# Kernel tuning notes

Measured on AMD Instinct MI355X. Metric: run time of the kernel, lower is better.

## Reference

```python
import jax, jax.numpy as jnp
import numpy as np

B, S, D = 2, 2048, 2048
H, KVH = 16, 4
HD = D // H          # 128 head dim
KVD = KVH * HD       # 512
BASE = 10000.0
EPS = 1.1920929e-07  # float32 eps, matches torch F.rms_norm default


def setup_inputs() -> dict:
    key = jax.random.key(0)
    ks = jax.random.split(key, 9)
    sd = 1.0 / np.sqrt(D)
    x = jax.random.normal(ks[0], (B, S, D), jnp.float32)
    Wq = jax.random.normal(ks[1], (D, D), jnp.float32) * sd
    bq = jnp.zeros((D,), jnp.float32)
    Wk = jax.random.normal(ks[2], (KVD, D), jnp.float32) * sd
    bk = jnp.zeros((KVD,), jnp.float32)
    Wv = jax.random.normal(ks[3], (KVD, D), jnp.float32) * sd
    bv = jnp.zeros((KVD,), jnp.float32)
    Wo = jax.random.normal(ks[4], (D, D), jnp.float32) * sd
    bo = jnp.zeros((D,), jnp.float32)
    q_gain = jnp.ones((H,), jnp.float32)
    return {"x": x, "Wq": Wq, "bq": bq, "Wk": Wk, "bk": bk,
            "Wv": Wv, "bv": bv, "Wo": Wo, "bo": bo, "q_gain": q_gain}


def _rms_norm(t):
    return t * jax.lax.rsqrt(jnp.mean(t * t, axis=-1, keepdims=True) + EPS)


def _rope_tables(s, dtype):
    inv_freq = 1.0 / (BASE ** (jnp.arange(0, HD, 2, dtype=jnp.float32) / HD))  # [HD/2]
    t = jnp.arange(s, dtype=jnp.float32)
    freqs = jnp.outer(t, inv_freq)                       # [s, HD/2]
    cos = jnp.cos(freqs)[None, None].astype(dtype)       # [1,1,s,HD/2]
    sin = jnp.sin(freqs)[None, None].astype(dtype)
    return cos, sin


def _apply_rope(t, cos, sin):
    half = t.shape[-1] // 2
    t1, t2 = t[..., :half], t[..., half:]
    return jnp.concatenate([t1 * cos + t2 * sin, -t1 * sin + t2 * cos], axis=-1)


def reference(x, Wq, bq, Wk, bk, Wv, bv, Wo, bo, q_gain):
    b, s, d = x.shape
    q = (jnp.einsum('bsd,ed->bse', x, Wq) + bq).reshape(b, s, H, HD).transpose(0, 2, 1, 3)
    k = (jnp.einsum('bsd,ed->bse', x, Wk) + bk).reshape(b, s, KVH, HD).transpose(0, 2, 1, 3)
    v = (jnp.einsum('bsd,ed->bse', x, Wv) + bv).reshape(b, s, KVH, HD).transpose(0, 2, 1, 3)
    # QK RMSNorm (no learned weight)
    q = _rms_norm(q)
    k = _rms_norm(k)
    # RoPE over full head dim (rope_dims=0 path)
    cos, sin = _rope_tables(s, q.dtype)
    q = _apply_rope(q, cos, sin)
    k = _apply_rope(k, cos, sin)
    # per-head gain on q
    q = q * q_gain[None, :, None, None]
    # GQA: repeat kv heads
    rep = H // KVH
    k = jnp.repeat(k, rep, axis=1)
    v = jnp.repeat(v, rep, axis=1)
    scale = HD ** -0.5
    attn = jnp.einsum('bhqd,bhkd->bhqk', q * scale, k)   # [b,H,s,s]
    causal = jnp.tril(jnp.ones((s, s), dtype=bool))
    attn = jnp.where(causal[None, None], attn, -jnp.inf)
    attn = jax.nn.softmax(attn, axis=-1)
    out = jnp.einsum('bhqk,bhkd->bqhd', attn, v).reshape(b, s, d)
    return jnp.einsum('bsd,ed->bse', out, Wo) + bo
```

## Files before the change

kernel.cpp:

```cpp
#include <hip/hip_runtime.h>
#include <hip/hip_bf16.h>

typedef __hip_bfloat16 bf16;
typedef unsigned short u16;
typedef short short8 __attribute__((ext_vector_type(8)));
typedef float f32x4  __attribute__((ext_vector_type(4)));

static __device__ __forceinline__ float ldf(const void* p, size_t i, int isbf16) {
    return isbf16 ? __bfloat162float(((const bf16*)p)[i]) : ((const float*)p)[i];
}
static __device__ __forceinline__ void stf(void* p, size_t i, float v, int isbf16) {
    if (isbf16) ((bf16*)p)[i] = __float2bfloat16(v);
    else        ((float*)p)[i] = v;
}

static __device__ __forceinline__ unsigned packf(float v) {
    unsigned ub = __float_as_uint(v);
    unsigned uh = ub & 0xFFFF0000u;
    float r = v - __uint_as_float(uh);
    return uh | (__float_as_uint(r) >> 16);
}
static __device__ __forceinline__ float unpackf(unsigned u) {
    return __uint_as_float(u & 0xFFFF0000u) + __uint_as_float(u << 16);
}

static __device__ __forceinline__ void upk8(uint4 a, uint4 b, short8& h, short8& l) {
    h = (short8){(short)(a.x >> 16), (short)(a.y >> 16), (short)(a.z >> 16), (short)(a.w >> 16),
                 (short)(b.x >> 16), (short)(b.y >> 16), (short)(b.z >> 16), (short)(b.w >> 16)};
    l = (short8){(short)(a.x), (short)(a.y), (short)(a.z), (short)(a.w),
                 (short)(b.x), (short)(b.y), (short)(b.z), (short)(b.w)};
}

static __device__ __forceinline__ void splitf8(float4 a, float4 b, short8& h, short8& l) {
    float vv[8] = {a.x, a.y, a.z, a.w, b.x, b.y, b.z, b.w};
    unsigned hh[8], ll[8];
#pragma unroll
    for (int j = 0; j < 8; j++) {
        unsigned ub = __float_as_uint(vv[j]);
        unsigned uh = ub & 0xFFFF0000u;
        float r = vv[j] - __uint_as_float(uh);
        hh[j] = uh >> 16;
        ll[j] = __float_as_uint(r) >> 16;
    }
    h = (short8){(short)hh[0], (short)hh[1], (short)hh[2], (short)hh[3],
                 (short)hh[4], (short)hh[5], (short)hh[6], (short)hh[7]};
    l = (short8){(short)ll[0], (short)ll[1], (short)ll[2], (short)ll[3],
                 (short)ll[4], (short)ll[5], (short)ll[6], (short)ll[7]};
}

static __device__ __forceinline__ float4 u2f4(uint4 a) {
    return (float4){__uint_as_float(a.x), __uint_as_float(a.y),
                    __uint_as_float(a.z), __uint_as_float(a.w)};
}
static __device__ __forceinline__ short8 u4_s8(uint4 a) {
    return (short8){(short)(a.x & 0xFFFF), (short)(a.x >> 16),
                    (short)(a.y & 0xFFFF), (short)(a.y >> 16),
                    (short)(a.z & 0xFFFF), (short)(a.z >> 16),
                    (short)(a.w & 0xFFFF), (short)(a.w >> 16)};
}

template<int AK>
static __device__ __forceinline__ void load_raw(const void* P, size_t e, int f, uint4* r) {
    if (AK == 1) {
        const uint4* p = (const uint4*)((const unsigned*)P + e);
        r[0] = p[0]; r[1] = p[1]; r[2] = p[2]; r[3] = p[3];
    } else if (f == 0) {
        const uint4* p = (const uint4*)((const float*)P + e);
        r[0] = p[0]; r[1] = p[1]; r[2] = p[2]; r[3] = p[3];
    } else {
        const uint4* p = (const uint4*)((const u16*)P + e);
        r[0] = p[0]; r[1] = p[1];
        r[2] = (uint4){0, 0, 0, 0}; r[3] = (uint4){0, 0, 0, 0};
    }
}

template<int AK>
static __device__ __forceinline__ void conv_raw(const uint4* r, int f,
        short8& h0, short8& h1, short8& l0, short8& l1) {
    if (AK == 1) {
        upk8(r[0], r[1], h0, l0);
        upk8(r[2], r[3], h1, l1);
    } else if (f == 0) {
        splitf8(u2f4(r[0]), u2f4(r[1]), h0, l0);
        splitf8(u2f4(r[2]), u2f4(r[3]), h1, l1);
    } else {
        h0 = u4_s8(r[0]); h1 = u4_s8(r[1]);
        l0 = (short8){0,0,0,0,0,0,0,0};
        l1 = (short8){0,0,0,0,0,0,0,0};
    }
}

__global__ void detect_dtype(const unsigned short* __restrict__ x, int n, int* __restrict__ flag)
{
    __shared__ int cnt;
    if (threadIdx.x == 0) cnt = 0;
    __syncthreads();
    int local = 0;
    for (int i = threadIdx.x; i < n; i += blockDim.x) {
        const unsigned int e = (x[i] >> 7) & 0xFF;
        if (e >= 134u) local++;
    }
    atomicAdd(&cnt, local);
    __syncthreads();
    if (threadIdx.x == 0) *flag = (cnt >= 32) ? 0 : 1;
}

template<int AK, int OUT, int BROW>
static __device__ __forceinline__ void gemm_core(
    const void* __restrict__ A, const void* __restrict__ W,
    const void* __restrict__ bias, void* __restrict__ C,
    int M, int N, int K, int f, int bx, int by, u16* sm)
{
    u16* Ah = sm;
    u16* Al = sm + 4096;
    u16* Wh = sm + 8192;
    u16* Wl = sm + 12288;

    const int t = threadIdx.x;
    const int w = t >> 6, lane = t & 63;
    const int wm = w >> 1, wn = w & 1;
    const int lr = lane & 15, quad = lane >> 4;
    const int bm = by * 128, bn = bx * 128;
    const int srow = t >> 1;
    const int scol = (t & 1) * 16;

    f32x4 acc[4][4];
#pragma unroll
    for (int i = 0; i < 4; i++)
#pragma unroll
        for (int j = 0; j < 4; j++) acc[i][j] = (f32x4){0.f, 0.f, 0.f, 0.f};

    uint4 ar[4], wr2[4];
    const size_t abase = (size_t)(bm + srow) * K + scol;
    const size_t wbase = (size_t)(bn + srow) * K + scol;
    load_raw<AK>(A, abase, f, ar);
    load_raw<0>(W, wbase, f, wr2);

    for (int k0 = 0; k0 < K; k0 += 32) {
        __syncthreads();
        {
            short8 h0, h1, l0, l1;
            conv_raw<AK>(ar, f, h0, h1, l0, l1);
            const int o = srow * 32 + scol;
            *(short8*)&Ah[o] = h0; *(short8*)&Ah[o + 8] = h1;
            *(short8*)&Al[o] = l0; *(short8*)&Al[o + 8] = l1;
            conv_raw<0>(wr2, f, h0, h1, l0, l1);
            *(short8*)&Wh[o] = h0; *(short8*)&Wh[o + 8] = h1;
            *(short8*)&Wl[o] = l0; *(short8*)&Wl[o + 8] = l1;
        }
        __syncthreads();
        if (k0 + 32 < K) {
            load_raw<AK>(A, abase + k0 + 32, f, ar);
            load_raw<0>(W, wbase + k0 + 32, f, wr2);
        }

        short8 avh[4], avl[4], bvh[4], bvl[4];
#pragma unroll
        for (int i = 0; i < 4; i++) {
            const int o = (wm * 64 + i * 16 + lr) * 32 + quad * 8;
            avh[i] = *(const short8*)&Ah[o];
            avl[i] = *(const short8*)&Al[o];
        }
#pragma unroll
        for (int j = 0; j < 4; j++) {
            const int o = (wn * 64 + j * 16 + lr) * 32 + quad * 8;
            bvh[j] = *(const short8*)&Wh[o];
            bvl[j] = *(const short8*)&Wl[o];
        }
        __builtin_amdgcn_s_setprio(1);
#pragma unroll
        for (int i = 0; i < 4; i++)
#pragma unroll
            for (int j = 0; j < 4; j++) {
                acc[i][j] = __builtin_amdgcn_mfma_f32_16x16x32_bf16(avl[i], bvh[j], acc[i][j], 0, 0, 0);
                acc[i][j] = __builtin_amdgcn_mfma_f32_16x16x32_bf16(avh[i], bvl[j], acc[i][j], 0, 0, 0);
                acc[i][j] = __builtin_amdgcn_mfma_f32_16x16x32_bf16(avh[i], bvh[j], acc[i][j], 0, 0, 0);
            }
        __builtin_amdgcn_s_setprio(0);
    }

#pragma unroll
    for (int j = 0; j < 4; j++) {
        const int col = bn + wn * 64 + j * 16 + lr;
        const float bc = BROW ? 0.f : ldf(bias, col, f);
#pragma unroll
        for (int i = 0; i < 4; i++) {
            const int row0 = bm + wm * 64 + i * 16 + quad * 4;
#pragma unroll
            for (int r = 0; r < 4; r++) {
                const int row = row0 + r;
                const float bb = BROW ? ldf(bias, row, f) : bc;
                const float val = acc[i][j][r] + bb;
                if (OUT == 1) ((unsigned*)C)[(size_t)row * N + col] = packf(val);
                else          stf(C, (size_t)row * N + col, val, f);
            }
        }
    }
}

template<int AK, int OUT, int BROW>
__global__ __launch_bounds__(256, 2)
void gemm3(const void* __restrict__ A, const void* __restrict__ W,
           const void* __restrict__ bias, void* __restrict__ C,
           int M, int N, int K, const int* __restrict__ flagp)
{
    extern __shared__ u16 sm[];
    gemm_core<AK, OUT, BROW>(A, W, bias, C, M, N, K, *flagp, blockIdx.x, blockIdx.y, sm);
}

__global__ __launch_bounds__(256, 2)
void gemm_kv(const void* __restrict__ x,
             const void* __restrict__ Wk, const void* __restrict__ bk, unsigned* __restrict__ Kp,
             const void* __restrict__ Wv, const void* __restrict__ bv, unsigned* __restrict__ Vtp,
             const int* __restrict__ flagp)
{
    extern __shared__ u16 sm[];
    const int f = *flagp;
    if (blockIdx.x < 4)
        gemm_core<0, 1, 0>(x, Wk, bk, Kp, 4096, 512, 2048, f, blockIdx.x, blockIdx.y, sm);
    else
        gemm_core<0, 1, 1>(Wv, x, bv, Vtp, 512, 4096, 2048, f, blockIdx.y, blockIdx.x - 4, sm);
}

__global__ __launch_bounds__(64)
void norm_rope_pk(unsigned* __restrict__ buf, const void* __restrict__ gain,
                  int nheads, float scale, const int* __restrict__ flagp)
{
    const int id = blockIdx.x;
    const int h  = id % nheads;
    const int bs = id / nheads;
    const int s  = bs & 2047;
    unsigned* v = buf + (size_t)bs * nheads * 128 + h * 128;
    const int i = threadIdx.x;

    float t1 = unpackf(v[i]);
    float t2 = unpackf(v[i + 64]);
    float ss = t1 * t1 + t2 * t2;
#pragma unroll
    for (int off = 32; off >= 1; off >>= 1) ss += __shfl_xor(ss, off);
    const float r = rsqrtf(ss * (1.0f / 128.0f) + 1.1920929e-07f);
    t1 *= r; t2 *= r;

    const float inv_freq = exp2f(-(float)i * 0.20762050593046014f);
    const float ph = (float)s * inv_freq;
    float sn, cs;
    __sincosf(ph, &sn, &cs);

    float g = scale;
    if (gain) g *= ldf(gain, h, *flagp);

    v[i]      = packf((t1 * cs + t2 * sn) * g);
    v[i + 64] = packf((-t1 * sn + t2 * cs) * g);
}

__global__ __launch_bounds__(256, 2)
void attn3(const unsigned* __restrict__ Qp, const unsigned* __restrict__ Kp,
           const unsigned* __restrict__ Vtp, unsigned* __restrict__ Cp)
{
    const int S = 2048, D = 2048, KVD = 512, MT = 4096;

    __shared__ __align__(16) u16 Kh[64 * 128], Kl[64 * 128];
    __shared__ __align__(16) u16 Vh[128 * 64], Vl[128 * 64];
    __shared__ __align__(16) u16 Ps[4][16][72];

    const int t = threadIdx.x, w = t >> 6, lane = t & 63;
    const int lr = lane & 15, quad = lane >> 4;
    const int h = blockIdx.y, b = blockIdx.z;
    const int kvh = h >> 2;

    const int qt0 = blockIdx.x;
    const int qt1 = 31 - blockIdx.x;
    const int nt0 = qt0 + 1, nt1 = qt1 + 1;
    const int total = nt0 + nt1;

    const int kr = t >> 2, kq = t & 3;
    const int vd = t >> 1, vh2 = t & 1;
    const unsigned* kg = Kp + (size_t)(b * S + kr) * KVD + kvh * 128 + kq * 32;
    const unsigned* vg = Vtp + (size_t)(kvh * 128 + vd) * MT + b * S + vh2 * 32;
    char* KhB = (char*)Kh; char* KlB = (char*)Kl;
    char* VhB = (char*)Vh; char* VlB = (char*)Vl;

    uint4 kv[8], vv[8];
#define ISSUE_KV(K0)                                                     \
    do {                                                                 \
        _Pragma("unroll")                                                \
        for (int u = 0; u < 8; u++) {                                    \
            kv[u] = *(const uint4*)(kg + (size_t)(K0) * KVD + u * 4);    \
            vv[u] = *(const uint4*)(vg + (K0) + u * 4);                  \
        }                                                                \
    } while (0)

    short8 qh[4], ql[4];
    f32x4 acc[8];
    float mreg[4], lreg[4];
    int q0 = 0, nt = nt0;

    ISSUE_KV(0);

    for (int it = 0; it < total; it++) {
        const int item = (it >= nt0) ? 1 : 0;
        const int kt = item ? (it - nt0) : it;
        if (kt == 0) {
            nt = item ? nt1 : nt0;
            q0 = (item ? qt1 : qt0) * 64;
            const unsigned* qs = Qp + (size_t)(b * S + q0 + w * 16 + lr) * D + h * 128;
#pragma unroll
            for (int kk = 0; kk < 4; kk++) {
                const uint4* p = (const uint4*)(qs + kk * 32 + quad * 8);
                upk8(p[0], p[1], qh[kk], ql[kk]);
            }
#pragma unroll
            for (int dt = 0; dt < 8; dt++) acc[dt] = (f32x4){0.f, 0.f, 0.f, 0.f};
#pragma unroll
            for (int r = 0; r < 4; r++) { mreg[r] = -1e30f; lreg[r] = 0.f; }
        }
        const int k0 = kt * 64;

        __syncthreads();
#pragma unroll
        for (int u2 = 0; u2 < 4; u2++) {
            short8 hh, ll;
            upk8(kv[2 * u2], kv[2 * u2 + 1], hh, ll);
            const int ko = (kr * 256 + kq * 64 + u2 * 16) ^ ((kr & 7) << 4);
            *(short8*)(KhB + ko) = hh;
            *(short8*)(KlB + ko) = ll;
            upk8(vv[2 * u2], vv[2 * u2 + 1], hh, ll);
            const int vo = (vd * 128 + vh2 * 64 + u2 * 16) ^ ((vd & 7) << 4);
            *(short8*)(VhB + vo) = hh;
            *(short8*)(VlB + vo) = ll;
        }
        __syncthreads();

        if (it + 1 < total) {
            const int nk0 = (it + 1 >= nt0) ? (it + 1 - nt0) * 64 : (it + 1) * 64;
            ISSUE_KV(nk0);
        }

        f32x4 sacc[4];
#pragma unroll
        for (int ct = 0; ct < 4; ct++) sacc[ct] = (f32x4){0.f, 0.f, 0.f, 0.f};
#pragma unroll
        for (int ks = 0; ks < 4; ks++) {
            short8 kbh[4], kbl[4];
#pragma unroll
            for (int ct = 0; ct < 4; ct++) {
                const int row = ct * 16 + lr;
                const int off = (row * 256 + ks * 64 + quad * 16) ^ ((row & 7) << 4);
                kbh[ct] = *(const short8*)(KhB + off);
                kbl[ct] = *(const short8*)(KlB + off);
            }
            __builtin_amdgcn_s_setprio(1);
#pragma unroll
            for (int ct = 0; ct < 4; ct++) {
                sacc[ct] = __builtin_amdgcn_mfma_f32_16x16x32_bf16(ql[ks], kbh[ct], sacc[ct], 0, 0, 0);
                sacc[ct] = __builtin_amdgcn_mfma_f32_16x16x32_bf16(qh[ks], kbl[ct], sacc[ct], 0, 0, 0);
                sacc[ct] = __builtin_amdgcn_mfma_f32_16x16x32_bf16(qh[ks], kbh[ct], sacc[ct], 0, 0, 0);
            }
            __builtin_amdgcn_s_setprio(0);
        }

        const bool diag = (kt == nt - 1);
        float p[4][4];
#pragma unroll
        for (int r = 0; r < 4; r++) {
            const int qg = q0 + w * 16 + quad * 4 + r;
            float s0 = sacc[0][r], s1 = sacc[1][r], s2 = sacc[2][r], s3 = sacc[3][r];
            if (diag) {
                if (k0 +  0 + lr > qg) s0 = -1e30f;
                if (k0 + 16 + lr > qg) s1 = -1e30f;
                if (k0 + 32 + lr > qg) s2 = -1e30f;
                if (k0 + 48 + lr > qg) s3 = -1e30f;
            }
            float mt = fmaxf(fmaxf(s0, s1), fmaxf(s2, s3));
#pragma unroll
            for (int off = 1; off < 16; off <<= 1) mt = fmaxf(mt, __shfl_xor(mt, off));
            const float mnew  = fmaxf(mreg[r], mt);
            const float alpha = __expf(mreg[r] - mnew);
            p[r][0] = (s0 <= -1e29f) ? 0.f : __expf(s0 - mnew);
            p[r][1] = (s1 <= -1e29f) ? 0.f : __expf(s1 - mnew);
            p[r][2] = (s2 <= -1e29f) ? 0.f : __expf(s2 - mnew);
            p[r][3] = (s3 <= -1e29f) ? 0.f : __expf(s3 - mnew);
            float ps = p[r][0] + p[r][1] + p[r][2] + p[r][3];
#pragma unroll
            for (int off = 1; off < 16; off <<= 1) ps += __shfl_xor(ps, off);
            lreg[r] = lreg[r] * alpha + ps;
            mreg[r] = mnew;
#pragma unroll
            for (int dt = 0; dt < 8; dt++) acc[dt][r] *= alpha;
        }

#pragma unroll
        for (int r = 0; r < 4; r++)
#pragma unroll
            for (int ct = 0; ct < 4; ct++)
                Ps[w][quad * 4 + r][ct * 16 + lr] = (u16)(__float_as_uint(p[r][ct]) >> 16);
#pragma unroll
        for (int ks2 = 0; ks2 < 2; ks2++) {
            const short8 pa = *(const short8*)((const char*)&Ps[w][lr][0] + ks2 * 64 + quad * 16);
            __builtin_amdgcn_s_setprio(1);
#pragma unroll
            for (int dt = 0; dt < 8; dt++) {
                const int vrow = dt * 16 + lr;
                const int off = (vrow * 128 + ks2 * 64 + quad * 16) ^ ((vrow & 7) << 4);
                const short8 vbh = *(const short8*)(VhB + off);
                const short8 vbl = *(const short8*)(VlB + off);
                acc[dt] = __builtin_amdgcn_mfma_f32_16x16x32_bf16(pa, vbh, acc[dt], 0, 0, 0);
                acc[dt] = __builtin_amdgcn_mfma_f32_16x16x32_bf16(pa, vbl, acc[dt], 0, 0, 0);
            }
            __builtin_amdgcn_s_setprio(0);
        }
#pragma unroll
        for (int r = 0; r < 4; r++)
#pragma unroll
            for (int ct = 0; ct < 4; ct++) {
                const unsigned ub = __float_as_uint(p[r][ct]);
                const unsigned uh = ub & 0xFFFF0000u;
                const float rr = p[r][ct] - __uint_as_float(uh);
                Ps[w][quad * 4 + r][ct * 16 + lr] = (u16)(__float_as_uint(rr) >> 16);
            }
#pragma unroll
        for (int ks2 = 0; ks2 < 2; ks2++) {
            const short8 pa = *(const short8*)((const char*)&Ps[w][lr][0] + ks2 * 64 + quad * 16);
            __builtin_amdgcn_s_setprio(1);
#pragma unroll
            for (int dt = 0; dt < 8; dt++) {
                const int vrow = dt * 16 + lr;
                const int off = (vrow * 128 + ks2 * 64 + quad * 16) ^ ((vrow & 7) << 4);
                const short8 vbh = *(const short8*)(VhB + off);
                acc[dt] = __builtin_amdgcn_mfma_f32_16x16x32_bf16(pa, vbh, acc[dt], 0, 0, 0);
            }
            __builtin_amdgcn_s_setprio(0);
        }

        if (kt == nt - 1) {
#pragma unroll
            for (int r = 0; r < 4; r++) {
                const float inv = 1.0f / lreg[r];
                unsigned* dst = Cp + (size_t)(b * S + q0 + w * 16 + quad * 4 + r) * D + h * 128 + lr;
#pragma unroll
                for (int dt = 0; dt < 8; dt++)
                    dst[dt * 16] = packf(acc[dt][r] * inv);
            }
        }
    }
#undef ISSUE_KV
}

extern "C" void kernel_launch(void* const* d_in, const int* in_sizes, int n_in,
                              void* d_out, int out_size, void* d_ws, size_t ws_size,
                              hipStream_t stream)
{
    const void* x  = d_in[0];
    const void* Wq = d_in[1];
    const void* bq = d_in[2];
    const void* Wk = d_in[3];
    const void* bk = d_in[4];
    const void* Wv = d_in[5];
    const void* bv = d_in[6];
    const void* Wo = d_in[7];
    const void* bo = d_in[8];
    const void* qg = d_in[9];

    const int B = 2, S = 2048, D = 2048, H = 16, KVH = 4, KVD = 512;
    const int M = B * S;

    unsigned* Qp  = (unsigned*)d_ws;
    unsigned* Kp  = Qp + (size_t)M * D;
    unsigned* Vtp = Kp + (size_t)M * KVD;
    unsigned* Cp  = Vtp + (size_t)KVD * M;
    int* flag = (int*)(Cp + (size_t)M * D);

    detect_dtype<<<1, 256, 0, stream>>>((const unsigned short*)x, 16384, flag);

    gemm3<0, 1, 0><<<dim3(D / 128, M / 128), 256, 32768, stream>>>(
        x, Wq, bq, Qp, M, D, D, flag);
    gemm_kv<<<dim3(8, 32), 256, 32768, stream>>>(x, Wk, bk, Kp, Wv, bv, Vtp, flag);

    norm_rope_pk<<<M * H, 64, 0, stream>>>(Qp, qg, H, 0.08838834764831845f, flag);
    norm_rope_pk<<<M * KVH, 64, 0, stream>>>(Kp, nullptr, KVH, 1.0f, flag);

    attn3<<<dim3(16, H, B), 256, 0, stream>>>(Qp, Kp, Vtp, Cp);

    gemm3<1, 2, 0><<<dim3(D / 128, M / 128), 256, 32768, stream>>>(
        Cp, Wo, bo, d_out, M, D, D, flag);
}
```

Before: 716.4 us.

## Pre-split activations into bf16 hi/lo planes and stream them with async LDS copies

Adds a split_x pass that converts x once into separate bf16 high and low planes. The Q, K and V projections are merged into one launch whose pre-split operand is copied straight into shared memory with global_load_lds, so it is no longer converted per tile in every block. K, V and the attention output are stored as planar hi/lo bf16 arrays instead of packed words, which lets attention and the output GEMM copy them without unpacking. This removes repeated fp32-to-bf16x2 splitting and register staging, at the cost of an extra pass over x and more workspace; the GEMMs now claim 3 blocks per SM through launch bounds.

Result: slower. 889.8 us (+24.2%).

```diff
diff --git a/kernel.cpp b/kernel.cpp
--- a/kernel.cpp
+++ b/kernel.cpp
@@ -5,6 +5,10 @@
 typedef unsigned short u16;
 typedef short short8 __attribute__((ext_vector_type(8)));
 typedef float f32x4  __attribute__((ext_vector_type(4)));
+
+static __device__ __forceinline__ float b2f(u16 u) {
+    union { unsigned int i; float f; } c; c.i = (unsigned int)u << 16; return c.f;
+}
 
 static __device__ __forceinline__ float ldf(const void* p, size_t i, int isbf16) {
     return isbf16 ? __bfloat162float(((const bf16*)p)[i]) : ((const float*)p)[i];
@@ -59,12 +63,8 @@
                     (short)(a.w & 0xFFFF), (short)(a.w >> 16)};
 }
 
-template<int AK>
 static __device__ __forceinline__ void load_raw(const void* P, size_t e, int f, uint4* r) {
-    if (AK == 1) {
-        const uint4* p = (const uint4*)((const unsigned*)P + e);
-        r[0] = p[0]; r[1] = p[1]; r[2] = p[2]; r[3] = p[3];
-    } else if (f == 0) {
+    if (f == 0) {
         const uint4* p = (const uint4*)((const float*)P + e);
         r[0] = p[0]; r[1] = p[1]; r[2] = p[2]; r[3] = p[3];
     } else {
@@ -73,14 +73,9 @@
         r[2] = (uint4){0, 0, 0, 0}; r[3] = (uint4){0, 0, 0, 0};
     }
 }
-
-template<int AK>
 static __device__ __forceinline__ void conv_raw(const uint4* r, int f,
         short8& h0, short8& h1, short8& l0, short8& l1) {
-    if (AK == 1) {
-        upk8(r[0], r[1], h0, l0);
-        upk8(r[2], r[3], h1, l1);
-    } else if (f == 0) {
+    if (f == 0) {
         splitf8(u2f4(r[0]), u2f4(r[1]), h0, l0);
         splitf8(u2f4(r[2]), u2f4(r[3]), h1, l1);
     } else {
@@ -88,6 +83,11 @@
         l0 = (short8){0,0,0,0,0,0,0,0};
         l1 = (short8){0,0,0,0,0,0,0,0};
     }
+}
+
+static __device__ __forceinline__ void async_copy16(const void* g, void* l) {
+    __builtin_amdgcn_global_load_lds((const __attribute__((address_space(1))) void*)g,
+                                     (__attribute__((address_space(3))) void*)l, 16, 0, 0);
 }
 
 __global__ void detect_dtype(const unsigned short* __restrict__ x, int n, int* __restrict__ flag)
@@ -105,24 +105,44 @@
     if (threadIdx.x == 0) *flag = (cnt >= 32) ? 0 : 1;
 }
 
-template<int AK, int OUT, int BROW>
+__global__ __launch_bounds__(256)
+void split_x(const void* __restrict__ x, u16* __restrict__ Xh, u16* __restrict__ Xl,
+             const int* __restrict__ flagp)
+{
+    const int f = *flagp;
+    const size_t i = ((size_t)blockIdx.x * 256 + threadIdx.x) * 8;
+    if (f == 0) {
+        const float4* p = (const float4*)((const float*)x + i);
+        short8 h, l;
+        splitf8(p[0], p[1], h, l);
+        *(short8*)(Xh + i) = h;
+        *(short8*)(Xl + i) = l;
+    } else {
+        *(short8*)(Xh + i) = *(const short8*)((const u16*)x + i);
+        *(short8*)(Xl + i) = (short8){0,0,0,0,0,0,0,0};
+    }
+}
+
+template<int AP, int BP, int OUT, int BROW>
 static __device__ __forceinline__ void gemm_core(
-    const void* __restrict__ A, const void* __restrict__ W,
-    const void* __restrict__ bias, void* __restrict__ C,
-    int M, int N, int K, int f, int bx, int by, u16* sm)
-{
-    u16* Ah = sm;
-    u16* Al = sm + 4096;
-    u16* Wh = sm + 8192;
-    u16* Wl = sm + 12288;
+    const void* __restrict__ Aa, const void* __restrict__ Ab,
+    const void* __restrict__ Ba, const void* __restrict__ Bb,
+    const void* __restrict__ bias, void* __restrict__ Ca, void* __restrict__ Cb,
+    int N, int K, int f, int bx, int by, u16* sm)
+{
+    u16* AhT = sm;
+    u16* AlT = sm + 4096;
+    u16* WhT = sm + 8192;
+    u16* WlT = sm + 12288;
 
     const int t = threadIdx.x;
     const int w = t >> 6, lane = t & 63;
     const int wm = w >> 1, wn = w & 1;
     const int lr = lane & 15, quad = lane >> 4;
     const int bm = by * 128, bn = bx * 128;
-    const int srow = t >> 1;
-    const int scol = (t & 1) * 16;
+    const int arow = lane >> 2;
+    const int acol = (lane & 3) * 8;
+    const int srow = t >> 1, scol = (t & 1) * 16;
 
     f32x4 acc[4][4];
 #pragma unroll
@@ -130,42 +150,54 @@
 #pragma unroll
         for (int j = 0; j < 4; j++) acc[i][j] = (f32x4){0.f, 0.f, 0.f, 0.f};
 
-    uint4 ar[4], wr2[4];
-    const size_t abase = (size_t)(bm + srow) * K + scol;
-    const size_t wbase = (size_t)(bn + srow) * K + scol;
-    load_raw<AK>(A, abase, f, ar);
-    load_raw<0>(W, wbase, f, wr2);
+    uint4 rr[4];
+    const void* rawP = AP ? Ba : Aa;
+    const size_t rawBase = AP ? ((size_t)(bn + srow) * K + scol)
+                              : ((size_t)(bm + srow) * K + scol);
+    load_raw(rawP, rawBase, f, rr);
 
     for (int k0 = 0; k0 < K; k0 += 32) {
         __syncthreads();
+        if (AP) {
+#pragma unroll
+            for (int c = 2 * w; c < 2 * w + 2; c++) {
+                const int row = c * 16 + arow;
+                async_copy16((const u16*)Aa + (size_t)(bm + row) * K + k0 + acol, &AhT[c * 512]);
+                async_copy16((const u16*)Ab + (size_t)(bm + row) * K + k0 + acol, &AlT[c * 512]);
+            }
+        }
+        if (BP) {
+#pragma unroll
+            for (int c = 2 * w; c < 2 * w + 2; c++) {
+                const int row = c * 16 + arow;
+                async_copy16((const u16*)Ba + (size_t)(bn + row) * K + k0 + acol, &WhT[c * 512]);
+                async_copy16((const u16*)Bb + (size_t)(bn + row) * K + k0 + acol, &WlT[c * 512]);
+            }
+        }
         {
             short8 h0, h1, l0, l1;
-            conv_raw<AK>(ar, f, h0, h1, l0, l1);
+            conv_raw(rr, f, h0, h1, l0, l1);
+            u16* H = AP ? WhT : AhT;
+            u16* L = AP ? WlT : AlT;
             const int o = srow * 32 + scol;
-            *(short8*)&Ah[o] = h0; *(short8*)&Ah[o + 8] = h1;
-            *(short8*)&Al[o] = l0; *(short8*)&Al[o + 8] = l1;
-            conv_raw<0>(wr2, f, h0, h1, l0, l1);
-            *(short8*)&Wh[o] = h0; *(short8*)&Wh[o + 8] = h1;
-            *(short8*)&Wl[o] = l0; *(short8*)&Wl[o + 8] = l1;
+            *(short8*)&H[o] = h0; *(short8*)&H[o + 8] = h1;
+            *(short8*)&L[o] = l0; *(short8*)&L[o + 8] = l1;
         }
         __syncthreads();
-        if (k0 + 32 < K) {
-            load_raw<AK>(A, abase + k0 + 32, f, ar);
-            load_raw<0>(W, wbase + k0 + 32, f, wr2);
-        }
+        if (k0 + 32 < K) load_raw(rawP, rawBase + k0 + 32, f, rr);
 
         short8 avh[4], avl[4], bvh[4], bvl[4];
 #pragma unroll
         for (int i = 0; i < 4; i++) {
             const int o = (wm * 64 + i * 16 + lr) * 32 + quad * 8;
-            avh[i] = *(const short8*)&Ah[o];
-            avl[i] = *(const short8*)&Al[o];
+            avh[i] = *(const short8*)&AhT[o];
+            avl[i] = *(const short8*)&AlT[o];
         }
 #pragma unroll
         for (int j = 0; j < 4; j++) {
             const int o = (wn * 64 + j * 16 + lr) * 32 + quad * 8;
-            bvh[j] = *(const short8*)&Wh[o];
-            bvl[j] = *(const short8*)&Wl[o];
+            bvh[j] = *(const short8*)&WhT[o];
+            bvl[j] = *(const short8*)&WlT[o];
         }
         __builtin_amdgcn_s_setprio(1);
 #pragma unroll
@@ -191,35 +223,54 @@
                 const int row = row0 + r;
                 const float bb = BROW ? ldf(bias, row, f) : bc;
                 const float val = acc[i][j][r] + bb;
-                if (OUT == 1) ((unsigned*)C)[(size_t)row * N + col] = packf(val);
-                else          stf(C, (size_t)row * N + col, val, f);
-            }
-        }
-    }
-}
-
-template<int AK, int OUT, int BROW>
-__global__ __launch_bounds__(256, 2)
-void gemm3(const void* __restrict__ A, const void* __restrict__ W,
-           const void* __restrict__ bias, void* __restrict__ C,
-           int M, int N, int K, const int* __restrict__ flagp)
-{
-    extern __shared__ u16 sm[];
-    gemm_core<AK, OUT, BROW>(A, W, bias, C, M, N, K, *flagp, blockIdx.x, blockIdx.y, sm);
-}
-
-__global__ __launch_bounds__(256, 2)
-void gemm_kv(const void* __restrict__ x,
-             const void* __restrict__ Wk, const void* __restrict__ bk, unsigned* __restrict__ Kp,
-             const void* __restrict__ Wv, const void* __restrict__ bv, unsigned* __restrict__ Vtp,
-             const int* __restrict__ flagp)
-{
-    extern __shared__ u16 sm[];
+                const size_t idx = (size_t)row * N + col;
+                if (OUT == 1)      ((unsigned*)Ca)[idx] = packf(val);
+                else if (OUT == 2) stf(Ca, idx, val, f);
+                else {
+                    const unsigned ub = __float_as_uint(val);
+                    const unsigned uh = ub & 0xFFFF0000u;
+                    ((u16*)Ca)[idx] = (u16)(uh >> 16);
+                    ((u16*)Cb)[idx] = (u16)(__float_as_uint(val - __uint_as_float(uh)) >> 16);
+                }
+            }
+        }
+    }
+}
+
+__global__ __launch_bounds__(256, 3)
+void gemm_qkv(const u16* __restrict__ Xh, const u16* __restrict__ Xl,
+              const void* __restrict__ Wq, const void* __restrict__ bq, unsigned* __restrict__ Qp,
+              const void* __restrict__ Wk, const void* __restrict__ bk,
+              u16* __restrict__ Khg, u16* __restrict__ Klg,
+              const void* __restrict__ Wv, const void* __restrict__ bv,
+              u16* __restrict__ Vthg, u16* __restrict__ Vtlg,
+              const int* __restrict__ flagp)
+{
+    __shared__ __align__(16) u16 sm[16384];
     const int f = *flagp;
-    if (blockIdx.x < 4)
-        gemm_core<0, 1, 0>(x, Wk, bk, Kp, 4096, 512, 2048, f, blockIdx.x, blockIdx.y, sm);
-    else
-        gemm_core<0, 1, 1>(Wv, x, bv, Vtp, 512, 4096, 2048, f, blockIdx.y, blockIdx.x - 4, sm);
+    const int id = blockIdx.x;
+    if (id < 512) {
+        gemm_core<1, 0, 1, 0>(Xh, Xl, Wq, nullptr, bq, Qp, nullptr,
+                              2048, 2048, f, id & 15, id >> 4, sm);
+    } else if (id < 640) {
+        const int v = id - 512;
+        gemm_core<1, 0, 3, 0>(Xh, Xl, Wk, nullptr, bk, Khg, Klg,
+                              512, 2048, f, v & 3, v >> 2, sm);
+    } else {
+        const int v = id - 640;
+        gemm_core<0, 1, 3, 1>(Wv, nullptr, Xh, Xl, bv, Vthg, Vtlg,
+                              4096, 2048, f, v >> 2, v & 3, sm);
+    }
+}
+
+__global__ __launch_bounds__(256, 3)
+void gemm_o(const u16* __restrict__ Ch, const u16* __restrict__ Cl,
+            const void* __restrict__ Wo, const void* __restrict__ bo,
+            void* __restrict__ out, const int* __restrict__ flagp)
+{
+    __shared__ __align__(16) u16 sm[16384];
+    gemm_core<1, 0, 2, 0>(Ch, Cl, Wo, nullptr, bo, out, nullptr,
+                          2048, 2048, *flagp, blockIdx.x & 15, blockIdx.x >> 4, sm);
 }
 
 __global__ __launch_bounds__(64)
@@ -253,9 +304,46 @@
     v[i + 64] = packf((-t1 * sn + t2 * cs) * g);
 }
 
+__global__ __launch_bounds__(64)
+void norm_rope_pl(u16* __restrict__ bh, u16* __restrict__ bl, int nheads)
+{
+    const int id = blockIdx.x;
+    const int h  = id % nheads;
+    const int bs = id / nheads;
+    const int s  = bs & 2047;
+    const size_t base = (size_t)bs * nheads * 128 + h * 128;
+    u16* ph = bh + base;
+    u16* pl = bl + base;
+    const int i = threadIdx.x;
+
+    float t1 = b2f(ph[i]) + b2f(pl[i]);
+    float t2 = b2f(ph[i + 64]) + b2f(pl[i + 64]);
+    float ss = t1 * t1 + t2 * t2;
+#pragma unroll
+    for (int off = 32; off >= 1; off >>= 1) ss += __shfl_xor(ss, off);
+    const float r = rsqrtf(ss * (1.0f / 128.0f) + 1.1920929e-07f);
+    t1 *= r; t2 *= r;
+
+    const float inv_freq = exp2f(-(float)i * 0.20762050593046014f);
+    const float phs = (float)s * inv_freq;
+    float sn, cs;
+    __sincosf(phs, &sn, &cs);
+
+    const float o1 = t1 * cs + t2 * sn;
+    const float o2 = -t1 * sn + t2 * cs;
+    unsigned u1 = __float_as_uint(o1) & 0xFFFF0000u;
+    unsigned u2 = __float_as_uint(o2) & 0xFFFF0000u;
+    ph[i]      = (u16)(u1 >> 16);
+    pl[i]      = (u16)(__float_as_uint(o1 - __uint_as_float(u1)) >> 16);
+    ph[i + 64] = (u16)(u2 >> 16);
+    pl[i + 64] = (u16)(__float_as_uint(o2 - __uint_as_float(u2)) >> 16);
+}
+
 __global__ __launch_bounds__(256, 2)
-void attn3(const unsigned* __restrict__ Qp, const unsigned* __restrict__ Kp,
-           const unsigned* __restrict__ Vtp, unsigned* __restrict__ Cp)
+void attn3(const unsigned* __restrict__ Qp,
+           const u16* __restrict__ Khg, const u16* __restrict__ Klg,
+           const u16* __restrict__ Vthg, const u16* __restrict__ Vtlg,
+           u16* __restrict__ Chg, u16* __restrict__ Clg)
 {
     const int S = 2048, D = 2048, KVD = 512, MT = 4096;
 
@@ -275,19 +363,25 @@
 
     const int kr = t >> 2, kq = t & 3;
     const int vd = t >> 1, vh2 = t & 1;
-    const unsigned* kg = Kp + (size_t)(b * S + kr) * KVD + kvh * 128 + kq * 32;
-    const unsigned* vg = Vtp + (size_t)(kvh * 128 + vd) * MT + b * S + vh2 * 32;
+    const size_t koff = (size_t)(b * S + kr) * KVD + kvh * 128 + kq * 32;
+    const size_t voff = (size_t)(kvh * 128 + vd) * MT + b * S + vh2 * 32;
+    const u16* khg = Khg + koff;
+    const u16* klg = Klg + koff;
+    const u16* vhg = Vthg + voff;
+    const u16* vlg = Vtlg + voff;
     char* KhB = (char*)Kh; char* KlB = (char*)Kl;
     char* VhB = (char*)Vh; char* VlB = (char*)Vl;
 
-    uint4 kv[8], vv[8];
-#define ISSUE_KV(K0)                                                     \
-    do {                                                                 \
-        _Pragma("unroll")                                                \
-        for (int u = 0; u < 8; u++) {                                    \
-            kv[u] = *(const uint4*)(kg + (size_t)(K0) * KVD + u * 4);    \
-            vv[u] = *(const uint4*)(vg + (K0) + u * 4);                  \
-        }                                                                \
+    uint4 khr[4], klr[4], vhr[4], vlr[4];
+#define ISSUE_KV(K0)                                                      \
+    do {                                                                  \
+        _Pragma("unroll")                                                 \
+        for (int u = 0; u < 4; u++) {                                     \
+            khr[u] = *(const uint4*)(khg + (size_t)(K0) * KVD + u * 8);   \
+            klr[u] = *(const uint4*)(klg + (size_t)(K0) * KVD + u * 8);   \
+            vhr[u] = *(const uint4*)(vhg + (K0) + u * 8);                 \
+            vlr[u] = *(const uint4*)(vlg + (K0) + u * 8);                 \
+        }                                                                 \
     } while (0)
 
     short8 qh[4], ql[4];
@@ -319,15 +413,12 @@
         __syncthreads();
 #pragma unroll
         for (int u2 = 0; u2 < 4; u2++) {
-            short8 hh, ll;
-            upk8(kv[2 * u2], kv[2 * u2 + 1], hh, ll);
             const int ko = (kr * 256 + kq * 64 + u2 * 16) ^ ((kr & 7) << 4);
-            *(short8*)(KhB + ko) = hh;
-            *(short8*)(KlB + ko) = ll;
-            upk8(vv[2 * u2], vv[2 * u2 + 1], hh, ll);
+            *(uint4*)(KhB + ko) = khr[u2];
+            *(uint4*)(KlB + ko) = klr[u2];
             const int vo = (vd * 128 + vh2 * 64 + u2 * 16) ^ ((vd & 7) << 4);
-            *(short8*)(VhB + vo) = hh;
-            *(short8*)(VlB + vo) = ll;
+            *(uint4*)(VhB + vo) = vhr[u2];
+            *(uint4*)(VlB + vo) = vlr[u2];
         }
         __syncthreads();
 
@@ -436,10 +527,15 @@
 #pragma unroll
             for (int r = 0; r < 4; r++) {
                 const float inv = 1.0f / lreg[r];
-                unsigned* dst = Cp + (size_t)(b * S + q0 + w * 16 + quad * 4 + r) * D + h * 128 + lr;
-#pragma unroll
-                for (int dt = 0; dt < 8; dt++)
-                    dst[dt * 16] = packf(acc[dt][r] * inv);
+                const size_t base = (size_t)(b * S + q0 + w * 16 + quad * 4 + r) * D + h * 128 + lr;
+#pragma unroll
+                for (int dt = 0; dt < 8; dt++) {
+                    const float val = acc[dt][r] * inv;
+                    const unsigned ub = __float_as_uint(val);
+                    const unsigned uh = ub & 0xFFFF0000u;
+                    Chg[base + dt * 16] = (u16)(uh >> 16);
+                    Clg[base + dt * 16] = (u16)(__float_as_uint(val - __uint_as_float(uh)) >> 16);
+                }
             }
         }
     }
@@ -464,23 +560,27 @@
     const int B = 2, S = 2048, D = 2048, H = 16, KVH = 4, KVD = 512;
     const int M = B * S;
 
-    unsigned* Qp  = (unsigned*)d_ws;
-    unsigned* Kp  = Qp + (size_t)M * D;
-    unsigned* Vtp = Kp + (size_t)M * KVD;
-    unsigned* Cp  = Vtp + (size_t)KVD * M;
-    int* flag = (int*)(Cp + (size_t)M * D);
+    unsigned* Qp = (unsigned*)d_ws;
+    u16* Khg  = (u16*)(Qp + (size_t)M * D);
+    u16* Klg  = Khg + (size_t)M * KVD;
+    u16* Vthg = Klg + (size_t)M * KVD;
+    u16* Vtlg = Vthg + (size_t)M * KVD;
+    u16* CXh  = Vtlg + (size_t)M * KVD;
+    u16* CXl  = CXh + (size_t)M * D;
+    int* flag = (int*)(CXl + (size_t)M * D);
 
     detect_dtype<<<1, 256, 0, stream>>>((const unsigned short*)x, 16384, flag);
 
-    gemm3<0, 1, 0><<<dim3(D / 128, M / 128), 256, 32768, stream>>>(
-        x, Wq, bq, Qp, M, D, D, flag);
-    gemm_kv<<<dim3(8, 32), 256, 32768, stream>>>(x, Wk, bk, Kp, Wv, bv, Vtp, flag);
+    split_x<<<(M * D) / (256 * 8), 256, 0, stream>>>(x, CXh, CXl, flag);
+
+    gemm_qkv<<<768, 256, 0, stream>>>(CXh, CXl, Wq, bq, Qp,
+                                      Wk, bk, Khg, Klg,
+                                      Wv, bv, Vthg, Vtlg, flag);
 
     norm_rope_pk<<<M * H, 64, 0, stream>>>(Qp, qg, H, 0.08838834764831845f, flag);
-    norm_rope_pk<<<M * KVH, 64, 0, stream>>>(Kp, nullptr, KVH, 1.0f, flag);
-
-    attn3<<<dim3(16, H, B), 256, 0, stream>>>(Qp, Kp, Vtp, Cp);
-
-    gemm3<1, 2, 0><<<dim3(D / 128, M / 128), 256, 32768, stream>>>(
-        Cp, Wo, bo, d_out, M, D, D, flag);
-}
+    norm_rope_pl<<<M * KVH, 64, 0, stream>>>(Khg, Klg, KVH);
+
+    attn3<<<dim3(16, H, B), 256, 0, stream>>>(Qp, Khg, Klg, Vthg, Vtlg, CXh, CXl);
+
+    gemm_o<<<512, 256, 0, stream>>>(CXh, CXl, Wo, bo, d_out, flag);
+}
```

## Pre-split x into bf16 hi/lo and stream GEMM tiles via async LDS loads

Applied to the files above, without the earlier changes.

A new split_x kernel converts x into separate bf16 high and low planes once, stored in the attention-output workspace. The Q, K and V projections now read those planes and copy them straight into LDS with global_load_lds, instead of re-splitting fp32 in every tile. Q, K and V are merged into one 768-block launch with a 3-blocks-per-CU launch bound, and the output GEMM gets its own specialised kernel. The cost is an extra pass writing the split x. The async tile loads are issued inside the same iteration that consumes them, so the register prefetch overlap is lost for those operands.

Result: faster. 673.6 us (-6.0%).

```diff
diff --git a/kernel.cpp b/kernel.cpp
--- a/kernel.cpp
+++ b/kernel.cpp
@@ -5,6 +5,10 @@
 typedef unsigned short u16;
 typedef short short8 __attribute__((ext_vector_type(8)));
 typedef float f32x4  __attribute__((ext_vector_type(4)));
+
+static __device__ __forceinline__ float b2f(u16 u) {
+    union { unsigned int i; float f; } c; c.i = (unsigned int)u << 16; return c.f;
+}
 
 static __device__ __forceinline__ float ldf(const void* p, size_t i, int isbf16) {
     return isbf16 ? __bfloat162float(((const bf16*)p)[i]) : ((const float*)p)[i];
@@ -59,9 +63,9 @@
                     (short)(a.w & 0xFFFF), (short)(a.w >> 16)};
 }
 
-template<int AK>
-static __device__ __forceinline__ void load_raw(const void* P, size_t e, int f, uint4* r) {
-    if (AK == 1) {
+template<int MODE>
+static __device__ __forceinline__ void load_any(const void* P, size_t e, int f, uint4* r) {
+    if (MODE == 2) {
         const uint4* p = (const uint4*)((const unsigned*)P + e);
         r[0] = p[0]; r[1] = p[1]; r[2] = p[2]; r[3] = p[3];
     } else if (f == 0) {
@@ -73,11 +77,10 @@
         r[2] = (uint4){0, 0, 0, 0}; r[3] = (uint4){0, 0, 0, 0};
     }
 }
-
-template<int AK>
-static __device__ __forceinline__ void conv_raw(const uint4* r, int f,
+template<int MODE>
+static __device__ __forceinline__ void conv_any(const uint4* r, int f,
         short8& h0, short8& h1, short8& l0, short8& l1) {
-    if (AK == 1) {
+    if (MODE == 2) {
         upk8(r[0], r[1], h0, l0);
         upk8(r[2], r[3], h1, l1);
     } else if (f == 0) {
@@ -90,6 +93,11 @@
     }
 }
 
+static __device__ __forceinline__ void async_copy16(const void* g, void* l) {
+    __builtin_amdgcn_global_load_lds((const __attribute__((address_space(1))) void*)g,
+                                     (__attribute__((address_space(3))) void*)l, 16, 0, 0);
+}
+
 __global__ void detect_dtype(const unsigned short* __restrict__ x, int n, int* __restrict__ flag)
 {
     __shared__ int cnt;
@@ -105,24 +113,44 @@
     if (threadIdx.x == 0) *flag = (cnt >= 32) ? 0 : 1;
 }
 
-template<int AK, int OUT, int BROW>
+__global__ __launch_bounds__(256)
+void split_x(const void* __restrict__ x, u16* __restrict__ Xh, u16* __restrict__ Xl,
+             const int* __restrict__ flagp)
+{
+    const int f = *flagp;
+    const size_t i = ((size_t)blockIdx.x * 256 + threadIdx.x) * 8;
+    if (f == 0) {
+        const float4* p = (const float4*)((const float*)x + i);
+        short8 h, l;
+        splitf8(p[0], p[1], h, l);
+        *(short8*)(Xh + i) = h;
+        *(short8*)(Xl + i) = l;
+    } else {
+        *(short8*)(Xh + i) = *(const short8*)((const u16*)x + i);
+        *(short8*)(Xl + i) = (short8){0,0,0,0,0,0,0,0};
+    }
+}
+
+template<int AM, int BM, int OUT, int BROW>
 static __device__ __forceinline__ void gemm_core(
-    const void* __restrict__ A, const void* __restrict__ W,
-    const void* __restrict__ bias, void* __restrict__ C,
-    int M, int N, int K, int f, int bx, int by, u16* sm)
-{
-    u16* Ah = sm;
-    u16* Al = sm + 4096;
-    u16* Wh = sm + 8192;
-    u16* Wl = sm + 12288;
+    const void* __restrict__ Aa, const void* __restrict__ Ab,
+    const void* __restrict__ Ba, const void* __restrict__ Bb,
+    const void* __restrict__ bias, void* __restrict__ Ca,
+    int N, int K, int f, int bx, int by, u16* sm)
+{
+    u16* AhT = sm;
+    u16* AlT = sm + 4096;
+    u16* WhT = sm + 8192;
+    u16* WlT = sm + 12288;
 
     const int t = threadIdx.x;
     const int w = t >> 6, lane = t & 63;
     const int wm = w >> 1, wn = w & 1;
     const int lr = lane & 15, quad = lane >> 4;
     const int bm = by * 128, bn = bx * 128;
-    const int srow = t >> 1;
-    const int scol = (t & 1) * 16;
+    const int arow = lane >> 2;
+    const int acol = (lane & 3) * 8;
+    const int srow = t >> 1, scol = (t & 1) * 16;
 
     f32x4 acc[4][4];
 #pragma unroll
@@ -130,42 +158,60 @@
 #pragma unroll
         for (int j = 0; j < 4; j++) acc[i][j] = (f32x4){0.f, 0.f, 0.f, 0.f};
 
-    uint4 ar[4], wr2[4];
-    const size_t abase = (size_t)(bm + srow) * K + scol;
-    const size_t wbase = (size_t)(bn + srow) * K + scol;
-    load_raw<AK>(A, abase, f, ar);
-    load_raw<0>(W, wbase, f, wr2);
+    uint4 ra[4], rb[4];
+    const size_t aBase = (size_t)(bm + srow) * K + scol;
+    const size_t bBase = (size_t)(bn + srow) * K + scol;
+    if (AM != 1) load_any<AM>(Aa, aBase, f, ra);
+    if (BM != 1) load_any<BM>(Ba, bBase, f, rb);
 
     for (int k0 = 0; k0 < K; k0 += 32) {
         __syncthreads();
-        {
+        if (AM == 1) {
+#pragma unroll
+            for (int c = 2 * w; c < 2 * w + 2; c++) {
+                const int row = c * 16 + arow;
+                async_copy16((const u16*)Aa + (size_t)(bm + row) * K + k0 + acol, &AhT[c * 512]);
+                async_copy16((const u16*)Ab + (size_t)(bm + row) * K + k0 + acol, &AlT[c * 512]);
+            }
+        } else {
             short8 h0, h1, l0, l1;
-            conv_raw<AK>(ar, f, h0, h1, l0, l1);
+            conv_any<AM>(ra, f, h0, h1, l0, l1);
             const int o = srow * 32 + scol;
-            *(short8*)&Ah[o] = h0; *(short8*)&Ah[o + 8] = h1;
-            *(short8*)&Al[o] = l0; *(short8*)&Al[o + 8] = l1;
-            conv_raw<0>(wr2, f, h0, h1, l0, l1);
-            *(short8*)&Wh[o] = h0; *(short8*)&Wh[o + 8] = h1;
-            *(short8*)&Wl[o] = l0; *(short8*)&Wl[o + 8] = l1;
+            *(short8*)&AhT[o] = h0; *(short8*)&AhT[o + 8] = h1;
+            *(short8*)&AlT[o] = l0; *(short8*)&AlT[o + 8] = l1;
+        }
+        if (BM == 1) {
+#pragma unroll
+            for (int c = 2 * w; c < 2 * w + 2; c++) {
+                const int row = c * 16 + arow;
+                async_copy16((const u16*)Ba + (size_t)(bn + row) * K + k0 + acol, &WhT[c * 512]);
+                async_copy16((const u16*)Bb + (size_t)(bn + row) * K + k0 + acol, &WlT[c * 512]);
+            }
+        } else {
+            short8 h0, h1, l0, l1;
+            conv_any<BM>(rb, f, h0, h1, l0, l1);
+            const int o = srow * 32 + scol;
+            *(short8*)&WhT[o] = h0; *(short8*)&WhT[o + 8] = h1;
+            *(short8*)&WlT[o] = l0; *(short8*)&WlT[o + 8] = l1;
         }
         __syncthreads();
         if (k0 + 32 < K) {
-            load_raw<AK>(A, abase + k0 + 32, f, ar);
-            load_raw<0>(W, wbase + k0 + 32, f, wr2);
+            if (AM != 1) load_any<AM>(Aa, aBase + k0 + 32, f, ra);
+            if (BM != 1) load_any<BM>(Ba, bBase + k0 + 32, f, rb);
         }
 
         short8 avh[4], avl[4], bvh[4], bvl[4];
 #pragma unroll
         for (int i = 0; i < 4; i++) {
             const int o = (wm * 64 + i * 16 + lr) * 32 + quad * 8;
-            avh[i] = *(const short8*)&Ah[o];
-            avl[i] = *(const short8*)&Al[o];
+            avh[i] = *(const short8*)&AhT[o];
+            avl[i] = *(const short8*)&AlT[o];
         }
 #pragma unroll
         for (int j = 0; j < 4; j++) {
             const int o = (wn * 64 + j * 16 + lr) * 32 + quad * 8;
-            bvh[j] = *(const short8*)&Wh[o];
-            bvl[j] = *(const short8*)&Wl[o];
+            bvh[j] = *(const short8*)&WhT[o];
+            bvl[j] = *(const short8*)&WlT[o];
         }
         __builtin_amdgcn_s_setprio(1);
 #pragma unroll
@@ -191,35 +237,46 @@
                 const int row = row0 + r;
                 const float bb = BROW ? ldf(bias, row, f) : bc;
                 const float val = acc[i][j][r] + bb;
-                if (OUT == 1) ((unsigned*)C)[(size_t)row * N + col] = packf(val);
-                else          stf(C, (size_t)row * N + col, val, f);
-            }
-        }
-    }
-}
-
-template<int AK, int OUT, int BROW>
+                const size_t idx = (size_t)row * N + col;
+                if (OUT == 1) ((unsigned*)Ca)[idx] = packf(val);
+                else          stf(Ca, idx, val, f);
+            }
+        }
+    }
+}
+
+__global__ __launch_bounds__(256, 3)
+void gemm_qkv(const u16* __restrict__ Xh, const u16* __restrict__ Xl,
+              const void* __restrict__ Wq, const void* __restrict__ bq, unsigned* __restrict__ Qp,
+              const void* __restrict__ Wk, const void* __restrict__ bk, unsigned* __restrict__ Kp,
+              const void* __restrict__ Wv, const void* __restrict__ bv, unsigned* __restrict__ Vtp,
+              const int* __restrict__ flagp)
+{
+    __shared__ __align__(16) u16 sm[16384];
+    const int f = *flagp;
+    const int id = blockIdx.x;
+    if (id < 512) {
+        gemm_core<1, 0, 1, 0>(Xh, Xl, Wq, nullptr, bq, Qp,
+                              2048, 2048, f, id & 15, id >> 4, sm);
+    } else if (id < 640) {
+        const int v = id - 512;
+        gemm_core<1, 0, 1, 0>(Xh, Xl, Wk, nullptr, bk, Kp,
+                              512, 2048, f, v & 3, v >> 2, sm);
+    } else {
+        const int v = id - 640;
+        gemm_core<0, 1, 1, 1>(Wv, nullptr, Xh, Xl, bv, Vtp,
+                              4096, 2048, f, v >> 2, v & 3, sm);
+    }
+}
+
 __global__ __launch_bounds__(256, 2)
-void gemm3(const void* __restrict__ A, const void* __restrict__ W,
-           const void* __restrict__ bias, void* __restrict__ C,
-           int M, int N, int K, const int* __restrict__ flagp)
-{
-    extern __shared__ u16 sm[];
-    gemm_core<AK, OUT, BROW>(A, W, bias, C, M, N, K, *flagp, blockIdx.x, blockIdx.y, sm);
-}
-
-__global__ __launch_bounds__(256, 2)
-void gemm_kv(const void* __restrict__ x,
-             const void* __restrict__ Wk, const void* __restrict__ bk, unsigned* __restrict__ Kp,
-             const void* __restrict__ Wv, const void* __restrict__ bv, unsigned* __restrict__ Vtp,
-             const int* __restrict__ flagp)
-{
-    extern __shared__ u16 sm[];
-    const int f = *flagp;
-    if (blockIdx.x < 4)
-        gemm_core<0, 1, 0>(x, Wk, bk, Kp, 4096, 512, 2048, f, blockIdx.x, blockIdx.y, sm);
-    else
-        gemm_core<0, 1, 1>(Wv, x, bv, Vtp, 512, 4096, 2048, f, blockIdx.y, blockIdx.x - 4, sm);
+void gemm_o(const unsigned* __restrict__ Cp, const void* __restrict__ Wo,
+            const void* __restrict__ bo, void* __restrict__ out,
+            const int* __restrict__ flagp)
+{
+    __shared__ __align__(16) u16 sm[16384];
+    gemm_core<2, 0, 2, 0>(Cp, nullptr, Wo, nullptr, bo, out,
+                          2048, 2048, *flagp, blockIdx.x & 15, blockIdx.x >> 4, sm);
 }
 
 __global__ __launch_bounds__(64)
@@ -469,18 +526,20 @@
     unsigned* Vtp = Kp + (size_t)M * KVD;
     unsigned* Cp  = Vtp + (size_t)KVD * M;
     int* flag = (int*)(Cp + (size_t)M * D);
+    u16* CXh = (u16*)Cp;
+    u16* CXl = CXh + (size_t)M * D;
 
     detect_dtype<<<1, 256, 0, stream>>>((const unsigned short*)x, 16384, flag);
 
-    gemm3<0, 1, 0><<<dim3(D / 128, M / 128), 256, 32768, stream>>>(
-        x, Wq, bq, Qp, M, D, D, flag);
-    gemm_kv<<<dim3(8, 32), 256, 32768, stream>>>(x, Wk, bk, Kp, Wv, bv, Vtp, flag);
+    split_x<<<(M * D) / (256 * 8), 256, 0, stream>>>(x, CXh, CXl, flag);
+
+    gemm_qkv<<<768, 256, 0, stream>>>(CXh, CXl, Wq, bq, Qp,
+                                      Wk, bk, Kp, Wv, bv, Vtp, flag);
 
     norm_rope_pk<<<M * H, 64, 0, stream>>>(Qp, qg, H, 0.08838834764831845f, flag);
     norm_rope_pk<<<M * KVH, 64, 0, stream>>>(Kp, nullptr, KVH, 1.0f, flag);
 
     attn3<<<dim3(16, H, B), 256, 0, stream>>>(Qp, Kp, Vtp, Cp);
 
-    gemm3<1, 2, 0><<<dim3(D / 128, M / 128), 256, 32768, stream>>>(
-        Cp, Wo, bo, d_out, M, D, D, flag);
-}
+    gemm_o<<<512, 256, 0, stream>>>(Cp, Wo, bo, d_out, flag);
+}
```
